# Kernel optimization log

Hardware: AMD Instinct MI355X
Metric: run time of the kernel (lower is better)

The kernel has to match this reference:

```python
import jax, jax.numpy as jnp
import numpy as np

N, E, DIN, H, C, ED = 50000, 500000, 264, 4, 32, 16
HID = H * C   # 128
OUT = 128
NEG_SLOPE = 0.2
LN_EPS = 1e-5


def _ln(x, g, b):
    mu = jnp.mean(x, axis=-1, keepdims=True)
    var = jnp.mean((x - mu) ** 2, axis=-1, keepdims=True)
    return (x - mu) * jax.lax.rsqrt(var + LN_EPS) * g + b


def _segment_softmax(scores, seg, num_segments):
    # scores: (E, H), seg: (E,) destination node ids
    m = jax.ops.segment_max(scores, seg, num_segments=num_segments)
    m = jnp.where(jnp.isfinite(m), m, 0.0)
    ex = jnp.exp(scores - m[seg])
    s = jax.ops.segment_sum(ex, seg, num_segments=num_segments)
    return ex / (s[seg] + 1e-16)


def _gatv2(x, src, dst, edge_attr, Wl, bl, Wr, br, We, att, bias):
    # GATv2Conv (PyG semantics): lin_l -> source, lin_r -> target, lin_edge (no bias)
    n = x.shape[0]
    xl = (x @ Wl + bl).reshape(n, H, C)          # source transform
    xr = (x @ Wr + br).reshape(n, H, C)          # target transform
    ee = (edge_attr @ We).reshape(-1, H, C)      # (E, H, C)
    m = xl[src] + xr[dst] + ee                   # per-edge pre-activation
    g = jnp.where(m > 0, m, NEG_SLOPE * m)       # leaky_relu(0.2)
    score = jnp.einsum('ehc,hc->eh', g, att)     # (E, H)
    alpha = _segment_softmax(score, dst, n)      # softmax over in-edges of each dst
    msg = xl[src] * alpha[..., None]             # (E, H, C)
    out = jax.ops.segment_sum(msg, dst, num_segments=n)
    return out.reshape(n, HID) + bias


def setup_inputs() -> dict:
    key = jax.random.key(0)
    ks = jax.random.split(key, 16)
    r = lambda k, s: jax.random.normal(k, s, dtype=jnp.float32) * 0.05
    return {
        'x': jax.random.normal(ks[0], (N, DIN), jnp.float32),
        'edge_attr': jax.random.normal(ks[1], (E, ED), jnp.float32),
        'Wl1': r(ks[2], (DIN, HID)), 'bl1': jnp.zeros((HID,), jnp.float32),
        'Wr1': r(ks[3], (DIN, HID)), 'br1': jnp.zeros((HID,), jnp.float32),
        'We1': r(ks[4], (ED, HID)), 'att1': r(ks[5], (H, C)), 'bias1': jnp.zeros((HID,), jnp.float32),
        'Wl2': r(ks[6], (HID, HID)), 'bl2': jnp.zeros((HID,), jnp.float32),
        'Wr2': r(ks[7], (HID, HID)), 'br2': jnp.zeros((HID,), jnp.float32),
        'We2': r(ks[8], (ED, HID)), 'att2': r(ks[9], (H, C)), 'bias2': jnp.zeros((HID,), jnp.float32),
        'Wres': r(ks[10], (DIN, HID)), 'bres': jnp.zeros((HID,), jnp.float32),
        'Wout': r(ks[11], (HID, OUT)), 'bout': jnp.zeros((OUT,), jnp.float32),
        'g1': jnp.ones((HID,), jnp.float32), 'bn1': jnp.zeros((HID,), jnp.float32),
        'g2': jnp.ones((HID,), jnp.float32), 'bn2': jnp.zeros((HID,), jnp.float32),
        'go': jnp.ones((OUT,), jnp.float32), 'bo': jnp.zeros((OUT,), jnp.float32),
        'edge_index': jax.random.randint(ks[12], (2, E), 0, N, dtype=jnp.int32),
    }


def reference(x, edge_attr, Wl1, bl1, Wr1, br1, We1, att1, bias1,
              Wl2, bl2, Wr2, br2, We2, att2, bias2,
              Wres, bres, Wout, bout, g1, bn1, g2, bn2, go, bo, edge_index):
    src, dst = edge_index[0], edge_index[1]
    residual = x @ Wres + bres
    h = _gatv2(x, src, dst, edge_attr, Wl1, bl1, Wr1, br1, We1, att1, bias1)
    h = jax.nn.elu(h)
    h = _ln(h + residual, g1, bn1)
    residual = h
    h = _gatv2(h, src, dst, edge_attr, Wl2, bl2, Wr2, br2, We2, att2, bias2)
    h = jax.nn.elu(h)
    h = _ln(h + residual, g2, bn2)
    context = _ln(h @ Wout + bout, go, bo)
    return context
```

## Files before the change

### kernel.cpp

```cpp
#include <hip/hip_runtime.h>
#include <hip/hip_bf16.h>
#include <math.h>
#include <stdint.h>

#define NN 50000
#define NE 500000
#define DIN 264
#define KP1 288
#define HID 128
#define EDIM 16

typedef __attribute__((ext_vector_type(8))) short short8;
typedef __attribute__((ext_vector_type(4))) float f32x4;

__device__ __forceinline__ short f2bf(float v) {
    union { float f; unsigned u; } x; x.f = v;
    unsigned r = x.u + 0x7fff + ((x.u >> 16) & 1);
    return (short)(r >> 16);
}
__device__ __forceinline__ float bf2f(short v) {
    union { float f; unsigned u; } x;
    x.u = ((unsigned)(unsigned short)v) << 16;
    return x.f;
}
__device__ __forceinline__ float bflo(unsigned u) {
    union { float f; unsigned u; } x; x.u = u << 16; return x.f;
}
__device__ __forceinline__ float bfhi(unsigned u) {
    union { float f; unsigned u; } x; x.u = u & 0xffff0000u; return x.f;
}
__device__ __forceinline__ unsigned pk2bf(float a, float b) {
    return (unsigned)(unsigned short)f2bf(a) | ((unsigned)(unsigned short)f2bf(b) << 16);
}

__device__ __forceinline__ void gload_lds16(const void* g, void* l) {
    __builtin_amdgcn_global_load_lds(
        (const __attribute__((address_space(1))) unsigned int*)g,
        (__attribute__((address_space(3))) unsigned int*)l, 16, 0, 0);
}

__global__ void k_count(const int* __restrict__ dst, int* __restrict__ cnt) {
    int e = blockIdx.x * blockDim.x + threadIdx.x;
    if (e < NE) atomicAdd(&cnt[dst[e]], 1);
}

__global__ __launch_bounds__(256) void k_scan1(const int* __restrict__ cnt,
                                               int* __restrict__ off, int* __restrict__ bsum) {
    __shared__ int buf[256];
    int b = blockIdx.x, t = threadIdx.x;
    int i = b * 256 + t;
    int v = (i < NN) ? cnt[i] : 0;
    buf[t] = v; __syncthreads();
    for (int s = 1; s < 256; s <<= 1) {
        int u = (t >= s) ? buf[t - s] : 0; __syncthreads();
        buf[t] += u; __syncthreads();
    }
    if (i < NN) off[i + 1] = buf[t];
    if (t == 255) bsum[b] = buf[255];
}

__global__ void k_scan2(int* __restrict__ bsum, int nb) {
    __shared__ int buf[256];
    int t = threadIdx.x;
    int o = (t < nb) ? bsum[t] : 0;
    buf[t] = o; __syncthreads();
    for (int s = 1; s < 256; s <<= 1) {
        int u = (t >= s) ? buf[t - s] : 0; __syncthreads();
        buf[t] += u; __syncthreads();
    }
    if (t < nb) bsum[t] = buf[t] - o;
}

__global__ void k_scan3c(int* __restrict__ off, const int* __restrict__ bsum,
                         int* __restrict__ cur) {
    int j = blockIdx.x * 256 + threadIdx.x;
    if (j > NN) return;
    int v = (j == 0) ? 0 : off[j] + bsum[(j - 1) >> 8];
    off[j] = v;
    if (j < NN) cur[j] = v;
}

__global__ void k_scatter(const int* __restrict__ src, const int* __restrict__ dst,
                          int* __restrict__ cur, int2* __restrict__ csr_se) {
    int e = blockIdx.x * blockDim.x + threadIdx.x;
    if (e < NE) {
        int d = dst[e];
        int p = atomicAdd(&cur[d], 1);
        csr_se[p] = make_int2(src[e], e);
    }
}

__global__ void k_fill_dst(const int* __restrict__ off, int* __restrict__ dstp) {
    int i = blockIdx.x * 256 + threadIdx.x;
    if (i < NN) {
        int b0 = off[i], b1 = off[i + 1];
        for (int p = b0; p < b1; ++p) dstp[p] = i;
    }
}

__global__ void k_cvt_x(const float* __restrict__ x, short* __restrict__ xb) {
    int idx = blockIdx.x * 256 + threadIdx.x;
    if (idx >= NN * KP1) return;
    int i = idx / KP1, k = idx - i * KP1;
    xb[idx] = (k < DIN) ? f2bf(x[(size_t)i * DIN + k]) : (short)0;
}

__global__ void k_prep_w(const float* __restrict__ Wl1, const float* __restrict__ Wr1,
                         const float* __restrict__ Wres, const float* __restrict__ Wl2,
                         const float* __restrict__ Wr2, const float* __restrict__ Wout,
                         const float* __restrict__ bl1, const float* __restrict__ br1,
                         const float* __restrict__ bres, const float* __restrict__ bl2,
                         const float* __restrict__ br2,
                         const float* __restrict__ We1, const float* __restrict__ We2,
                         const float* __restrict__ att1, const float* __restrict__ att2,
                         short* __restrict__ Wt1, short* __restrict__ Wt2,
                         short* __restrict__ Wt3, float* __restrict__ bcat1,
                         float* __restrict__ bcat2,
                         short* __restrict__ WeT1, short* __restrict__ WeT2,
                         short* __restrict__ attB1, short* __restrict__ attB2) {
    int idx = blockIdx.x * 256 + threadIdx.x;
    if (idx < 384 * KP1) {
        int n = idx / KP1, k = idx - n * KP1;
        float v = 0.f;
        if (k < DIN) {
            const float* W = (n < 128) ? Wl1 : ((n < 256) ? Wr1 : Wres);
            v = W[(size_t)k * 128 + (n & 127)];
        }
        Wt1[idx] = f2bf(v);
        return;
    }
    idx -= 384 * KP1;
    if (idx < 256 * 128) {
        int n = idx >> 7, k = idx & 127;
        const float* W = (n < 128) ? Wl2 : Wr2;
        Wt2[idx] = f2bf(W[(size_t)k * 128 + (n & 127)]);
        return;
    }
    idx -= 256 * 128;
    if (idx < 128 * 128) {
        int n = idx >> 7, k = idx & 127;
        Wt3[idx] = f2bf(Wout[(size_t)k * 128 + n]);
        return;
    }
    idx -= 128 * 128;
    if (idx < 384) {
        bcat1[idx] = (idx < 128) ? bl1[idx] : ((idx < 256) ? br1[idx - 128] : bres[idx - 256]);
        return;
    }
    idx -= 384;
    if (idx < 256) {
        bcat2[idx] = (idx < 128) ? bl2[idx] : br2[idx - 128];
        return;
    }
    idx -= 256;
    if (idx < 128 * 32) {
        int n = idx >> 5, k = idx & 31;
        WeT1[idx] = (k < EDIM) ? f2bf(We1[(size_t)k * 128 + n]) : (short)0;
        return;
    }
    idx -= 128 * 32;
    if (idx < 128 * 32) {
        int n = idx >> 5, k = idx & 31;
        WeT2[idx] = (k < EDIM) ? f2bf(We2[(size_t)k * 128 + n]) : (short)0;
        return;
    }
    idx -= 128 * 32;
    if (idx < 16 * 128) {
        int n = idx >> 7, k = idx & 127;
        attB1[idx] = (n == (k >> 5)) ? f2bf(att1[k]) : (short)0;
        return;
    }
    idx -= 16 * 128;
    if (idx < 16 * 128) {
        int n = idx >> 7, k = idx & 127;
        attB2[idx] = (n == (k >> 5)) ? f2bf(att2[k]) : (short)0;
    }
}

__global__ __launch_bounds__(256) void k_gather_ea(const int2* __restrict__ csr_se,
                                                   const float* __restrict__ ea,
                                                   short* __restrict__ eaperm) {
    int pos = blockIdx.x * 256 + threadIdx.x;
    if (pos >= NE) return;
    int e = csr_se[pos].y;
    const float4* r = (const float4*)(ea + (size_t)e * EDIM);
    float4 v0 = r[0], v1 = r[1], v2 = r[2], v3 = r[3];
    uint4 w0 = make_uint4(pk2bf(v0.x, v0.y), pk2bf(v0.z, v0.w),
                          pk2bf(v1.x, v1.y), pk2bf(v1.z, v1.w));
    uint4 w1 = make_uint4(pk2bf(v2.x, v2.y), pk2bf(v2.z, v2.w),
                          pk2bf(v3.x, v3.y), pk2bf(v3.z, v3.w));
    uint4* o = (uint4*)(eaperm + (size_t)pos * 32);
    o[0] = w0; o[1] = w1;
    o[2] = make_uint4(0, 0, 0, 0);
    o[3] = make_uint4(0, 0, 0, 0);
}

template <bool BF16OUT>
__global__ __launch_bounds__(256) void k_mfma_gemm(const short* __restrict__ A,
                                                   const short* __restrict__ Bt,
                                                   const float* __restrict__ bias,
                                                   float* __restrict__ Cf,
                                                   short* __restrict__ Cb,
                                                   int M, int Kpad, int NS) {
    __shared__ short As[128 * 32];
    __shared__ short Bs[128 * 32];
    int t = threadIdx.x;
    int lane = t & 63, wid = t >> 6;
    int wm = (wid & 1) * 64, wn = (wid >> 1) * 64;
    int cl = lane & 15, quad = lane >> 4;
    int row0 = blockIdx.x * 128;
    int col0 = blockIdx.y * 128;

    f32x4 acc[4][4];
#pragma unroll
    for (int i = 0; i < 4; ++i)
#pragma unroll
        for (int j = 0; j < 4; ++j) acc[i][j] = (f32x4)0.f;

    for (int k0 = 0; k0 < Kpad; k0 += 32) {
#pragma unroll
        for (int r = 0; r < 2; ++r) {
            int c = t + r * 256;
            int m = c >> 2;
            int row = row0 + m; if (row >= M) row = M - 1;
            const char* ga = (const char*)A + ((size_t)row * Kpad + k0) * 2 + (c & 3) * 16;
            gload_lds16(ga, (char*)As + c * 16);
            int n = col0 + m;
            const char* gb = (const char*)Bt + ((size_t)n * Kpad + k0) * 2 + (c & 3) * 16;
            gload_lds16(gb, (char*)Bs + c * 16);
        }
        __syncthreads();

        short8 a[4], b[4];
#pragma unroll
        for (int mi = 0; mi < 4; ++mi)
            a[mi] = *(const short8*)&As[(wm + mi * 16 + cl) * 32 + quad * 8];
#pragma unroll
        for (int ni = 0; ni < 4; ++ni)
            b[ni] = *(const short8*)&Bs[(wn + ni * 16 + cl) * 32 + quad * 8];
#pragma unroll
        for (int mi = 0; mi < 4; ++mi)
#pragma unroll
            for (int ni = 0; ni < 4; ++ni)
                acc[mi][ni] = __builtin_amdgcn_mfma_f32_16x16x32_bf16(a[mi], b[ni], acc[mi][ni], 0, 0, 0);
        __syncthreads();
    }

#pragma unroll
    for (int mi = 0; mi < 4; ++mi)
#pragma unroll
        for (int ni = 0; ni < 4; ++ni) {
            int col = col0 + wn + ni * 16 + cl;
            float bv = bias[col];
#pragma unroll
            for (int r = 0; r < 4; ++r) {
                int row = row0 + wm + mi * 16 + quad * 4 + r;
                if (row < M) {
                    float v = acc[mi][ni][r] + bv;
                    if (BF16OUT) Cb[(size_t)row * NS + col] = f2bf(v);
                    else         Cf[(size_t)row * NS + col] = v;
                }
            }
        }
}

__global__ __launch_bounds__(256) void k_gemm_ln(const short* __restrict__ A,
                                                 const short* __restrict__ Bt,
                                                 const float* __restrict__ bias,
                                                 const float* __restrict__ gamma,
                                                 const float* __restrict__ beta,
                                                 float* __restrict__ out, int M) {
    __shared__ short As[128 * 32];
    __shared__ short Bs[128 * 32];
    __shared__ float redS[128][2];
    int t = threadIdx.x;
    int lane = t & 63, wid = t >> 6;
    int wm = (wid & 1) * 64, wn = (wid >> 1) * 64;
    int cl = lane & 15, quad = lane >> 4;
    int row0 = blockIdx.x * 128;
    int wh = wid >> 1;

    f32x4 acc[4][4];
#pragma unroll
    for (int i = 0; i < 4; ++i)
#pragma unroll
        for (int j = 0; j < 4; ++j) acc[i][j] = (f32x4)0.f;

    for (int k0 = 0; k0 < 128; k0 += 32) {
#pragma unroll
        for (int r = 0; r < 2; ++r) {
            int c = t + r * 256;
            int m = c >> 2;
            int row = row0 + m; if (row >= M) row = M - 1;
            const char* ga = (const char*)A + ((size_t)row * 128 + k0) * 2 + (c & 3) * 16;
            gload_lds16(ga, (char*)As + c * 16);
            const char* gb = (const char*)Bt + ((size_t)m * 128 + k0) * 2 + (c & 3) * 16;
            gload_lds16(gb, (char*)Bs + c * 16);
        }
        __syncthreads();

        short8 a[4], b[4];
#pragma unroll
        for (int mi = 0; mi < 4; ++mi)
            a[mi] = *(const short8*)&As[(wm + mi * 16 + cl) * 32 + quad * 8];
#pragma unroll
        for (int ni = 0; ni < 4; ++ni)
            b[ni] = *(const short8*)&Bs[(wn + ni * 16 + cl) * 32 + quad * 8];
#pragma unroll
        for (int mi = 0; mi < 4; ++mi)
#pragma unroll
            for (int ni = 0; ni < 4; ++ni)
                acc[mi][ni] = __builtin_amdgcn_mfma_f32_16x16x32_bf16(a[mi], b[ni], acc[mi][ni], 0, 0, 0);
        __syncthreads();
    }

    float bv[4], gv[4], bev[4];
#pragma unroll
    for (int ni = 0; ni < 4; ++ni) {
        int col = wn + ni * 16 + cl;
        bv[ni] = bias[col]; gv[ni] = gamma[col]; bev[ni] = beta[col];
    }

    float s[4][4];
#pragma unroll
    for (int mi = 0; mi < 4; ++mi)
#pragma unroll
        for (int r = 0; r < 4; ++r) {
            float v = (acc[mi][0][r] + bv[0]) + (acc[mi][1][r] + bv[1]) +
                      (acc[mi][2][r] + bv[2]) + (acc[mi][3][r] + bv[3]);
            v += __shfl_xor(v, 1, 64);
            v += __shfl_xor(v, 2, 64);
            v += __shfl_xor(v, 4, 64);
            v += __shfl_xor(v, 8, 64);
            s[mi][r] = v;
        }
    if (cl == 0) {
#pragma unroll
        for (int mi = 0; mi < 4; ++mi)
#pragma unroll
            for (int r = 0; r < 4; ++r)
                redS[wm + mi * 16 + quad * 4 + r][wh] = s[mi][r];
    }
    __syncthreads();
    float mean[4][4];
#pragma unroll
    for (int mi = 0; mi < 4; ++mi)
#pragma unroll
        for (int r = 0; r < 4; ++r) {
            int rl = wm + mi * 16 + quad * 4 + r;
            mean[mi][r] = (redS[rl][0] + redS[rl][1]) * (1.f / 128.f);
        }
    __syncthreads();

#pragma unroll
    for (int mi = 0; mi < 4; ++mi)
#pragma unroll
        for (int r = 0; r < 4; ++r) {
            float q = 0.f;
#pragma unroll
            for (int ni = 0; ni < 4; ++ni) {
                float d = acc[mi][ni][r] + bv[ni] - mean[mi][r];
                q = fmaf(d, d, q);
            }
            q += __shfl_xor(q, 1, 64);
            q += __shfl_xor(q, 2, 64);
            q += __shfl_xor(q, 4, 64);
            q += __shfl_xor(q, 8, 64);
            s[mi][r] = q;
        }
    if (cl == 0) {
#pragma unroll
        for (int mi = 0; mi < 4; ++mi)
#pragma unroll
            for (int r = 0; r < 4; ++r)
                redS[wm + mi * 16 + quad * 4 + r][wh] = s[mi][r];
    }
    __syncthreads();

#pragma unroll
    for (int mi = 0; mi < 4; ++mi)
#pragma unroll
        for (int r = 0; r < 4; ++r) {
            int rl = wm + mi * 16 + quad * 4 + r;
            int row = row0 + rl;
            if (row < M) {
                float rstd = rsqrtf((redS[rl][0] + redS[rl][1]) * (1.f / 128.f) + 1e-5f);
#pragma unroll
                for (int ni = 0; ni < 4; ++ni) {
                    int col = wn + ni * 16 + cl;
                    float d = acc[mi][ni][r] + bv[ni] - mean[mi][r];
                    out[(size_t)row * 128 + col] = fmaf(d * rstd, gv[ni], bev[ni]);
                }
            }
        }
}

template <int STRIDE>
__global__ __launch_bounds__(512) void k_edge_score(const short* __restrict__ eaperm,
                                                    const short* __restrict__ WeT,
                                                    const short* __restrict__ attB,
                                                    const int2* __restrict__ csr_se,
                                                    const int* __restrict__ dstp,
                                                    const short* __restrict__ C,
                                                    float* __restrict__ pe) {
    __shared__ short Gs[128 * 136];
    __shared__ short Ab[16 * 136];
    __shared__ int sS[128], sD[128];
    int t = threadIdx.x;
    int lane = t & 63, wid = t >> 6;
    int wm2 = (wid & 1) * 64;
    int wn2 = (wid >> 1) * 32;
    int cl = lane & 15, quad = lane >> 4;
    long e0 = (long)blockIdx.x * 128;

    if (t < 128) {
        long ep = e0 + t; if (ep >= NE) ep = NE - 1;
        sS[t] = csr_se[ep].x;
        sD[t] = dstp[ep];
    } else if (t < 384) {
        int u = t - 128;
        int rr = u >> 4, cc = (u & 15) * 8;
        *(short8*)&Ab[rr * 136 + cc] = *(const short8*)&attB[rr * 128 + cc];
    }

    short8 a[4], b[2];
#pragma unroll
    for (int mi = 0; mi < 4; ++mi) {
        long e = e0 + wm2 + mi * 16 + cl; if (e >= NE) e = NE - 1;
        a[mi] = *(const short8*)&eaperm[e * 32 + quad * 8];
    }
#pragma unroll
    for (int ni = 0; ni < 2; ++ni)
        b[ni] = *(const short8*)&WeT[(size_t)(wn2 + ni * 16 + cl) * 32 + quad * 8];

    f32x4 acc[4][2];
#pragma unroll
    for (int i = 0; i < 4; ++i) { acc[i][0] = (f32x4)0.f; acc[i][1] = (f32x4)0.f; }
#pragma unroll
    for (int mi = 0; mi < 4; ++mi)
#pragma unroll
        for (int ni = 0; ni < 2; ++ni)
            acc[mi][ni] = __builtin_amdgcn_mfma_f32_16x16x32_bf16(a[mi], b[ni], acc[mi][ni], 0, 0, 0);
    __syncthreads();

#pragma unroll
    for (int mi = 0; mi < 4; ++mi) {
#pragma unroll
        for (int r = 0; r < 4; ++r) {
            int eloc = wm2 + mi * 16 + quad * 4 + r;
            const short* xlr = C + (size_t)sS[eloc] * STRIDE;
            const short* xrr = C + (size_t)sD[eloc] * STRIDE + 128;
            int f0 = wn2 + cl, f1 = wn2 + 16 + cl;
            float xl0 = bf2f(xlr[f0]), xr0 = bf2f(xrr[f0]);
            float xl1 = bf2f(xlr[f1]), xr1 = bf2f(xrr[f1]);
            float g0 = acc[mi][0][r] + xl0 + xr0;
            float g1 = acc[mi][1][r] + xl1 + xr1;
            g0 = fmaxf(g0, 0.2f * g0);
            g1 = fmaxf(g1, 0.2f * g1);
            Gs[eloc * 136 + f0] = f2bf(g0);
            Gs[eloc * 136 + f1] = f2bf(g1);
        }
    }
    __syncthreads();

    f32x4 sacc = (f32x4)0.f;
    int em0 = wid * 16;
#pragma unroll
    for (int ks = 0; ks < 4; ++ks) {
        short8 ag = *(const short8*)&Gs[(em0 + cl) * 136 + ks * 32 + quad * 8];
        short8 bg = *(const short8*)&Ab[cl * 136 + ks * 32 + quad * 8];
        sacc = __builtin_amdgcn_mfma_f32_16x16x32_bf16(ag, bg, sacc, 0, 0, 0);
    }

    if (cl < 4) {
#pragma unroll
        for (int r = 0; r < 4; ++r) {
            long epos = e0 + em0 + quad * 4 + r;
            if (epos < NE) pe[epos * 4 + cl] = __expf(sacc[r]);
        }
    }
}

template <int STRIDE>
__global__ __launch_bounds__(256) void k_fused_agg(const int* __restrict__ off,
                                                   const int2* __restrict__ csr_se,
                                                   const float* __restrict__ pe,
                                                   const short* __restrict__ C,
                                                   const short* __restrict__ resid, int rstride,
                                                   const float* __restrict__ bias,
                                                   const float* __restrict__ gamma,
                                                   const float* __restrict__ beta,
                                                   short* __restrict__ outb) {
    int t = threadIdx.x;
    int w = t >> 6, l = t & 63;
    int f0 = (l >> 4) * 32 + (l & 15) * 2;
    int fp = f0 >> 1;
    int hd = l >> 4;

    float2 bs2 = ((const float2*)bias)[fp];
    float2 gv = ((const float2*)gamma)[fp];
    float2 bev = ((const float2*)beta)[fp];

    int n0 = (blockIdx.x * 4 + w) * 4;
    int nend = n0 + 4; if (nend > NN) nend = NN;

    for (int i = n0; i < nend; ++i) {
        unsigned rp = *(const unsigned*)&resid[(size_t)i * rstride + f0];
        int b0 = off[i], b1 = off[i + 1];

        float lA = 0.f, aA0 = 0.f, aA1 = 0.f;
        float lB = 0.f, aB0 = 0.f, aB1 = 0.f;
        int pos = b0;
        int sA = 0, sB = 0; float pA = 0.f, pB = 0.f;
        bool have = (pos + 2 <= b1);
        if (have) {
            sA = csr_se[pos].x; sB = csr_se[pos + 1].x;
            pA = pe[(size_t)pos * 4 + hd]; pB = pe[(size_t)(pos + 1) * 4 + hd];
        }
        while (have) {
            bool haven = (pos + 4 <= b1);
            int nsA = 0, nsB = 0; float npA = 0.f, npB = 0.f;
            if (haven) {
                nsA = csr_se[pos + 2].x; nsB = csr_se[pos + 3].x;
                npA = pe[(size_t)(pos + 2) * 4 + hd]; npB = pe[(size_t)(pos + 3) * 4 + hd];
            }
            unsigned xlA = *(const unsigned*)&C[(size_t)sA * STRIDE + f0];
            unsigned xlB = *(const unsigned*)&C[(size_t)sB * STRIDE + f0];
            lA += pA; lB += pB;
            aA0 = fmaf(pA, bflo(xlA), aA0);
            aA1 = fmaf(pA, bfhi(xlA), aA1);
            aB0 = fmaf(pB, bflo(xlB), aB0);
            aB1 = fmaf(pB, bfhi(xlB), aB1);
            pos += 2;
            sA = nsA; sB = nsB; pA = npA; pB = npB;
            have = haven;
        }
        if (pos < b1) {
            int s1 = csr_se[pos].x;
            float p1 = pe[(size_t)pos * 4 + hd];
            unsigned xlv = *(const unsigned*)&C[(size_t)s1 * STRIDE + f0];
            lA += p1;
            aA0 = fmaf(p1, bflo(xlv), aA0);
            aA1 = fmaf(p1, bfhi(xlv), aA1);
        }
        float l_run = lA + lB;
        float acc0 = aA0 + aB0, acc1 = aA1 + aB1;

        float inv = 1.f / (l_run + 1e-16f);
        float o0 = fmaf(acc0, inv, bs2.x);
        float o1 = fmaf(acc1, inv, bs2.y);
        o0 = o0 > 0.f ? o0 : (__expf(o0) - 1.f);
        o1 = o1 > 0.f ? o1 : (__expf(o1) - 1.f);
        float v0 = o0 + bflo(rp), v1 = o1 + bfhi(rp);
        float s = v0 + v1;
#pragma unroll
        for (int o = 32; o > 0; o >>= 1) s += __shfl_xor(s, o, 64);
        float mean = s * (1.f / 128.f);
        float d0 = v0 - mean, d1 = v1 - mean;
        float q = fmaf(d0, d0, d1 * d1);
#pragma unroll
        for (int o = 32; o > 0; o >>= 1) q += __shfl_xor(q, o, 64);
        float rstd = rsqrtf(q * (1.f / 128.f) + 1e-5f);
        float r0 = fmaf(d0 * rstd, gv.x, bev.x);
        float r1 = fmaf(d1 * rstd, gv.y, bev.y);
        unsigned op = (unsigned)(unsigned short)f2bf(r0) |
                      (((unsigned)(unsigned short)f2bf(r1)) << 16);
        *(unsigned*)&outb[(size_t)i * 128 + f0] = op;
    }
}

extern "C" void kernel_launch(void* const* d_in, const int* in_sizes, int n_in,
                              void* d_out, int out_size, void* d_ws, size_t ws_size,
                              hipStream_t stream) {
    (void)in_sizes; (void)n_in; (void)out_size; (void)ws_size;
    const float* x     = (const float*)d_in[0];
    const float* ea    = (const float*)d_in[1];
    const float* Wl1   = (const float*)d_in[2];
    const float* bl1   = (const float*)d_in[3];
    const float* Wr1   = (const float*)d_in[4];
    const float* br1   = (const float*)d_in[5];
    const float* We1   = (const float*)d_in[6];
    const float* att1  = (const float*)d_in[7];
    const float* bias1 = (const float*)d_in[8];
    const float* Wl2   = (const float*)d_in[9];
    const float* bl2   = (const float*)d_in[10];
    const float* Wr2   = (const float*)d_in[11];
    const float* br2   = (const float*)d_in[12];
    const float* We2   = (const float*)d_in[13];
    const float* att2  = (const float*)d_in[14];
    const float* bias2 = (const float*)d_in[15];
    const float* Wres  = (const float*)d_in[16];
    const float* bres  = (const float*)d_in[17];
    const float* Wout  = (const float*)d_in[18];
    const float* bout  = (const float*)d_in[19];
    const float* g1    = (const float*)d_in[20];
    const float* bn1   = (const float*)d_in[21];
    const float* g2    = (const float*)d_in[22];
    const float* bn2   = (const float*)d_in[23];
    const float* go    = (const float*)d_in[24];
    const float* bo    = (const float*)d_in[25];
    const int*   ei    = (const int*)d_in[26];
    const int* srcv = ei;
    const int* dstv = ei + NE;
    float* outp = (float*)d_out;

    char* p = (char*)d_ws;
    auto carve = [&](size_t bytes) {
        char* r = p;
        p += (bytes + 255) & ~(size_t)255;
        return r;
    };
    short* xb    = (short*)carve((size_t)NN * KP1 * 2);
    short* Wt1   = (short*)carve((size_t)384 * KP1 * 2);
    short* Wt2   = (short*)carve((size_t)256 * 128 * 2);
    short* Wt3   = (short*)carve((size_t)128 * 128 * 2);
    short* WeT1  = (short*)carve((size_t)128 * 32 * 2);
    short* WeT2  = (short*)carve((size_t)128 * 32 * 2);
    short* attB1 = (short*)carve((size_t)16 * 128 * 2);
    short* attB2 = (short*)carve((size_t)16 * 128 * 2);
    float* bcat1 = (float*)carve(384 * 4);
    float* bcat2 = (float*)carve(256 * 4);
    short* C1    = (short*)carve((size_t)NN * 384 * 2);
    short* h1b   = (short*)carve((size_t)NN * 128 * 2);
    short* h2b   = (short*)carve((size_t)NN * 128 * 2);
    int* off     = (int*)carve((size_t)(NN + 1) * 4);
    int* cur     = (int*)carve((size_t)NN * 4);
    int* bsum    = (int*)carve(256 * 4);
    int2* csr_se = (int2*)carve((size_t)NE * 8);
    int* dstp    = (int*)carve((size_t)NE * 4);
    short* eaperm = (short*)carve((size_t)NE * 32 * 2);
    float* pe    = (float*)carve((size_t)NE * 4 * 4);

    short* C2 = C1;

    const int NB = (NN + 255) / 256;

    hipMemsetAsync(cur, 0, (size_t)NN * 4, stream);
    k_count<<<(NE + 255) / 256, 256, 0, stream>>>(dstv, cur);
    k_scan1<<<NB, 256, 0, stream>>>(cur, off, bsum);
    k_scan2<<<1, 256, 0, stream>>>(bsum, NB);
    k_scan3c<<<(NN + 256) / 256, 256, 0, stream>>>(off, bsum, cur);
    k_scatter<<<(NE + 255) / 256, 256, 0, stream>>>(srcv, dstv, cur, csr_se);
    k_fill_dst<<<NB, 256, 0, stream>>>(off, dstp);

    k_cvt_x<<<((size_t)NN * KP1 + 255) / 256, 256, 0, stream>>>(x, xb);
    int prep_total = 384 * KP1 + 256 * 128 + 128 * 128 + 384 + 256 + 2 * 128 * 32 + 2 * 16 * 128;
    k_prep_w<<<(prep_total + 255) / 256, 256, 0, stream>>>(Wl1, Wr1, Wres, Wl2, Wr2, Wout,
                                                           bl1, br1, bres, bl2, br2,
                                                           We1, We2, att1, att2,
                                                           Wt1, Wt2, Wt3, bcat1, bcat2,
                                                           WeT1, WeT2, attB1, attB2);
    k_gather_ea<<<(NE + 255) / 256, 256, 0, stream>>>(csr_se, ea, eaperm);

    int mb  = (NN + 127) / 128;
    int ebk = (NE + 127) / 128;
    int gagg = (NN + 15) / 16;

    k_mfma_gemm<true><<<dim3(mb, 3), 256, 0, stream>>>(xb, Wt1, bcat1, nullptr, C1, NN, KP1, 384);
    k_edge_score<384><<<ebk, 512, 0, stream>>>(eaperm, WeT1, attB1, csr_se, dstp, C1, pe);
    k_fused_agg<384><<<gagg, 256, 0, stream>>>(off, csr_se, pe, C1,
                                               C1 + 256, 384, bias1, g1, bn1, h1b);
    k_mfma_gemm<true><<<dim3(mb, 2), 256, 0, stream>>>(h1b, Wt2, bcat2, nullptr, C2, NN, 128, 256);
    k_edge_score<256><<<ebk, 512, 0, stream>>>(eaperm, WeT2, attB2, csr_se, dstp, C2, pe);
    k_fused_agg<256><<<gagg, 256, 0, stream>>>(off, csr_se, pe, C2,
                                               h1b, 128, bias2, g2, bn2, h2b);
    k_gemm_ln<<<mb, 256, 0, stream>>>(h2b, Wt3, bout, go, bo, outp, NN);
}
```

Measured before the change: 481.6 us.

## Fuse CSR setup kernels and widen gather unroll in fused aggregation

Folds the in-degree count into the x-to-bf16 conversion kernel and the dst-index fill into the edge-attr gather kernel, removing two launches. The fused aggregation kernel now keeps four independent edge accumulators with prefetch of the next four, instead of two, and each wave handles 2 nodes rather than 4, doubling the grid. The aim is more memory-level parallelism in the gather-bound aggregation and less launch overhead, at the cost of more registers and a longer scalar tail loop for low-degree nodes. The grid is computed as NN/8, which relies on NN being divisible by 8.

```diff
diff --git a/kernel.cpp b/kernel.cpp
--- a/kernel.cpp
+++ b/kernel.cpp
@@ -37,11 +37,6 @@
     __builtin_amdgcn_global_load_lds(
         (const __attribute__((address_space(1))) unsigned int*)g,
         (__attribute__((address_space(3))) unsigned int*)l, 16, 0, 0);
-}
-
-__global__ void k_count(const int* __restrict__ dst, int* __restrict__ cnt) {
-    int e = blockIdx.x * blockDim.x + threadIdx.x;
-    if (e < NE) atomicAdd(&cnt[dst[e]], 1);
 }
 
 __global__ __launch_bounds__(256) void k_scan1(const int* __restrict__ cnt,
@@ -90,16 +85,10 @@
     }
 }
 
-__global__ void k_fill_dst(const int* __restrict__ off, int* __restrict__ dstp) {
-    int i = blockIdx.x * 256 + threadIdx.x;
-    if (i < NN) {
-        int b0 = off[i], b1 = off[i + 1];
-        for (int p = b0; p < b1; ++p) dstp[p] = i;
-    }
-}
-
-__global__ void k_cvt_x(const float* __restrict__ x, short* __restrict__ xb) {
+__global__ void k_cvt_x_count(const float* __restrict__ x, short* __restrict__ xb,
+                              const int* __restrict__ dst, int* __restrict__ cnt) {
     int idx = blockIdx.x * 256 + threadIdx.x;
+    if (idx < NE) atomicAdd(&cnt[dst[idx]], 1);
     if (idx >= NN * KP1) return;
     int i = idx / KP1, k = idx - i * KP1;
     xb[idx] = (k < DIN) ? f2bf(x[(size_t)i * DIN + k]) : (short)0;
@@ -179,8 +168,14 @@
 
 __global__ __launch_bounds__(256) void k_gather_ea(const int2* __restrict__ csr_se,
                                                    const float* __restrict__ ea,
-                                                   short* __restrict__ eaperm) {
+                                                   short* __restrict__ eaperm,
+                                                   const int* __restrict__ off,
+                                                   int* __restrict__ dstp) {
     int pos = blockIdx.x * 256 + threadIdx.x;
+    if (pos < NN) {
+        int b0 = off[pos], b1 = off[pos + 1];
+        for (int p = b0; p < b1; ++p) dstp[p] = pos;
+    }
     if (pos >= NE) return;
     int e = csr_se[pos].y;
     const float4* r = (const float4*)(ea + (size_t)e * EDIM);
@@ -501,50 +496,66 @@
     float2 gv = ((const float2*)gamma)[fp];
     float2 bev = ((const float2*)beta)[fp];
 
-    int n0 = (blockIdx.x * 4 + w) * 4;
-    int nend = n0 + 4; if (nend > NN) nend = NN;
+    int n0 = (blockIdx.x * 4 + w) * 2;
+    int nend = n0 + 2; if (nend > NN) nend = NN;
 
     for (int i = n0; i < nend; ++i) {
         unsigned rp = *(const unsigned*)&resid[(size_t)i * rstride + f0];
         int b0 = off[i], b1 = off[i + 1];
 
-        float lA = 0.f, aA0 = 0.f, aA1 = 0.f;
-        float lB = 0.f, aB0 = 0.f, aB1 = 0.f;
+        float lr[4] = {0.f, 0.f, 0.f, 0.f};
+        float a0[4] = {0.f, 0.f, 0.f, 0.f};
+        float a1[4] = {0.f, 0.f, 0.f, 0.f};
         int pos = b0;
-        int sA = 0, sB = 0; float pA = 0.f, pB = 0.f;
-        bool have = (pos + 2 <= b1);
+        int sC[4] = {0, 0, 0, 0};
+        float pC[4] = {0.f, 0.f, 0.f, 0.f};
+        bool have = (pos + 4 <= b1);
         if (have) {
-            sA = csr_se[pos].x; sB = csr_se[pos + 1].x;
-            pA = pe[(size_t)pos * 4 + hd]; pB = pe[(size_t)(pos + 1) * 4 + hd];
+#pragma unroll
+            for (int j = 0; j < 4; ++j) {
+                int2 se = csr_se[pos + j];
+                sC[j] = se.x;
+                pC[j] = pe[(size_t)(pos + j) * 4 + hd];
+            }
         }
         while (have) {
-            bool haven = (pos + 4 <= b1);
-            int nsA = 0, nsB = 0; float npA = 0.f, npB = 0.f;
+            bool haven = (pos + 8 <= b1);
+            int nS[4] = {0, 0, 0, 0};
+            float nP[4] = {0.f, 0.f, 0.f, 0.f};
             if (haven) {
-                nsA = csr_se[pos + 2].x; nsB = csr_se[pos + 3].x;
-                npA = pe[(size_t)(pos + 2) * 4 + hd]; npB = pe[(size_t)(pos + 3) * 4 + hd];
+#pragma unroll
+                for (int j = 0; j < 4; ++j) {
+                    int2 se = csr_se[pos + 4 + j];
+                    nS[j] = se.x;
+                    nP[j] = pe[(size_t)(pos + 4 + j) * 4 + hd];
+                }
             }
-            unsigned xlA = *(const unsigned*)&C[(size_t)sA * STRIDE + f0];
-            unsigned xlB = *(const unsigned*)&C[(size_t)sB * STRIDE + f0];
-            lA += pA; lB += pB;
-            aA0 = fmaf(pA, bflo(xlA), aA0);
-            aA1 = fmaf(pA, bfhi(xlA), aA1);
-            aB0 = fmaf(pB, bflo(xlB), aB0);
-            aB1 = fmaf(pB, bfhi(xlB), aB1);
-            pos += 2;
-            sA = nsA; sB = nsB; pA = npA; pB = npB;
+            unsigned xl[4];
+#pragma unroll
+            for (int j = 0; j < 4; ++j)
+                xl[j] = *(const unsigned*)&C[(size_t)sC[j] * STRIDE + f0];
+#pragma unroll
+            for (int j = 0; j < 4; ++j) {
+                lr[j] += pC[j];
+                a0[j] = fmaf(pC[j], bflo(xl[j]), a0[j]);
+                a1[j] = fmaf(pC[j], bfhi(xl[j]), a1[j]);
+            }
+            pos += 4;
+#pragma unroll
+            for (int j = 0; j < 4; ++j) { sC[j] = nS[j]; pC[j] = nP[j]; }
             have = haven;
         }
-        if (pos < b1) {
-            int s1 = csr_se[pos].x;
+        for (; pos < b1; ++pos) {
+            int2 se = csr_se[pos];
             float p1 = pe[(size_t)pos * 4 + hd];
-            unsigned xlv = *(const unsigned*)&C[(size_t)s1 * STRIDE + f0];
-            lA += p1;
-            aA0 = fmaf(p1, bflo(xlv), aA0);
-            aA1 = fmaf(p1, bfhi(xlv), aA1);
-        }
-        float l_run = lA + lB;
-        float acc0 = aA0 + aB0, acc1 = aA1 + aB1;
+            unsigned xlv = *(const unsigned*)&C[(size_t)se.x * STRIDE + f0];
+            lr[0] += p1;
+            a0[0] = fmaf(p1, bflo(xlv), a0[0]);
+            a1[0] = fmaf(p1, bfhi(xlv), a1[0]);
+        }
+        float l_run = (lr[0] + lr[1]) + (lr[2] + lr[3]);
+        float acc0 = (a0[0] + a0[1]) + (a0[2] + a0[3]);
+        float acc1 = (a1[0] + a1[1]) + (a1[2] + a1[3]);
 
         float inv = 1.f / (l_run + 1e-16f);
         float o0 = fmaf(acc0, inv, bs2.x);
@@ -636,25 +647,23 @@
     const int NB = (NN + 255) / 256;
 
     hipMemsetAsync(cur, 0, (size_t)NN * 4, stream);
-    k_count<<<(NE + 255) / 256, 256, 0, stream>>>(dstv, cur);
+    k_cvt_x_count<<<((size_t)NN * KP1 + 255) / 256, 256, 0, stream>>>(x, xb, dstv, cur);
     k_scan1<<<NB, 256, 0, stream>>>(cur, off, bsum);
     k_scan2<<<1, 256, 0, stream>>>(bsum, NB);
     k_scan3c<<<(NN + 256) / 256, 256, 0, stream>>>(off, bsum, cur);
     k_scatter<<<(NE + 255) / 256, 256, 0, stream>>>(srcv, dstv, cur, csr_se);
-    k_fill_dst<<<NB, 256, 0, stream>>>(off, dstp);
-
-    k_cvt_x<<<((size_t)NN * KP1 + 255) / 256, 256, 0, stream>>>(x, xb);
+
     int prep_total = 384 * KP1 + 256 * 128 + 128 * 128 + 384 + 256 + 2 * 128 * 32 + 2 * 16 * 128;
     k_prep_w<<<(prep_total + 255) / 256, 256, 0, stream>>>(Wl1, Wr1, Wres, Wl2, Wr2, Wout,
                                                            bl1, br1, bres, bl2, br2,
                                                            We1, We2, att1, att2,
                                                            Wt1, Wt2, Wt3, bcat1, bcat2,
                                                            WeT1, WeT2, attB1, attB2);
-    k_gather_ea<<<(NE + 255) / 256, 256, 0, stream>>>(csr_se, ea, eaperm);
+    k_gather_ea<<<(NE + 255) / 256, 256, 0, stream>>>(csr_se, ea, eaperm, off, dstp);
 
     int mb  = (NN + 127) / 128;
     int ebk = (NE + 127) / 128;
-    int gagg = (NN + 15) / 16;
+    int gagg = NN / 8;
 
     k_mfma_gemm<true><<<dim3(mb, 3), 256, 0, stream>>>(xb, Wt1, bcat1, nullptr, C1, NN, KP1, 384);
     k_edge_score<384><<<ebk, 512, 0, stream>>>(eaperm, WeT1, attB1, csr_se, dstp, C1, pe);
```

After: 460.4 us. 4.4% less time.
